# Kernel tuning notes

Hardware: AMD Instinct MI355X
Metric: run time of the kernel (lower is better)

Reference implementation:

```python
import jax, jax.numpy as jnp
import numpy as np
import math

N = 50000      # nodes (single node type 'mapping_var')
D = 128        # in_feats
R = 3          # relations
E = 800000     # edges per relation
OUT = 64
ALPHA = 0.5
BETA1 = math.log(2.0)    # log(lambda/layer + 1), layer=1, lambda=1
BETA2 = math.log(1.5)    # layer=2
SLOPE = 0.01             # leaky_relu default negative slope


def setup_inputs() -> dict:
    key = jax.random.key(0)
    ks = jax.random.split(key, 8)
    x = jax.random.normal(ks[0], (N, D), dtype=jnp.float32)
    src = jax.random.randint(ks[1], (R, E), 0, N, dtype=jnp.int32)
    dst = jax.random.randint(ks[2], (R, E), 0, N, dtype=jnp.int32)
    W1 = jax.random.normal(ks[3], (R, D, D), dtype=jnp.float32) * 0.05
    b1 = jnp.zeros((R, D), dtype=jnp.float32)
    W2 = jax.random.normal(ks[4], (R, D, D), dtype=jnp.float32) * 0.05
    b2 = jnp.zeros((R, D), dtype=jnp.float32)
    Wlin = jax.random.normal(ks[5], (D, OUT), dtype=jnp.float32) * 0.05
    blin = jnp.zeros((OUT,), dtype=jnp.float32)
    return {"x": x, "src": src, "dst": dst, "W1": W1, "b1": b1,
            "W2": W2, "b2": b2, "Wlin": Wlin, "blin": blin}


def _gcn2_rel(h, feat0, src, dst, W, b, beta, act):
    """One GCN2Conv on one relation. h,feat0: [N,D]; src,dst: [E]."""
    ones = jnp.ones(src.shape, h.dtype)
    deg_out = jnp.maximum(jax.ops.segment_sum(ones, src, num_segments=N), 1.0)
    deg_in = jnp.maximum(jax.ops.segment_sum(ones, dst, num_segments=N), 1.0)
    hs = h * (deg_out ** -0.5)[:, None]              # src-side normalize
    agg = jax.ops.segment_sum(hs[src], dst, num_segments=N)  # SpMM via gather+scatter
    feat = agg * (deg_in ** -0.5)[:, None]           # dst-side normalize
    rst = feat * (1.0 - ALPHA) + ALPHA * feat0       # initial-residual blend
    rst = (1.0 - beta) * rst + beta * (rst @ W) + b  # identity mapping (project_initial_features)
    if act:
        rst = jnp.where(rst >= 0, rst, SLOPE * rst)  # leaky_relu
    return rst


def reference(x, src, dst, W1, b1, W2, b2, Wlin, blin):
    # conv1: per-relation GCN2Conv(layer=1, leaky_relu), mean-aggregate over relations
    h1 = jax.vmap(lambda s, d, w, bb: _gcn2_rel(x, x, s, d, w, bb, BETA1, True))(
        src, dst, W1, b1).mean(axis=0)
    # dropout: eval-mode identity
    # conv2: per-relation GCN2Conv(layer=2, no activation), feat_0 = original inputs
    h2 = jax.vmap(lambda s, d, w, bb: _gcn2_rel(h1, x, s, d, w, bb, BETA2, False))(
        src, dst, W2, b2).mean(axis=0)
    return h2 @ Wlin + blin
```

## Files before the change

### kernel.cpp

```cpp
#include <hip/hip_runtime.h>

#define NN    50000
#define DD    128
#define RR    3
#define EE    800000
#define OUTD  64
#define BKT   128
#define NBK   391
#define CAP   2560
#define CAPB  2560
#define CHUNK 2048
#define NCH   391
#define NPB   3125
#define ALPHA_ 0.5f
#define SLOPE_ 0.01f
#define BETA1_ 0.6931471805599453f
#define BETA2_ 0.4054651081081644f

typedef __attribute__((ext_vector_type(8))) short short8;
typedef __attribute__((ext_vector_type(4))) float f32x4;

__device__ __forceinline__ unsigned short f2b(float f) {
    unsigned int u = __builtin_bit_cast(unsigned int, f);
    u += 0x7FFFu + ((u >> 16) & 1u);
    return (unsigned short)(u >> 16);
}
__device__ __forceinline__ unsigned int pack2(float lo, float hi) {
    return (unsigned int)f2b(lo) | ((unsigned int)f2b(hi) << 16);
}
__device__ __forceinline__ float blo(unsigned int w) { return __builtin_bit_cast(float, w << 16); }
__device__ __forceinline__ float bhi(unsigned int w) { return __builtin_bit_cast(float, w & 0xFFFF0000u); }

__global__ __launch_bounds__(256) void bin_kernel(
    const int* __restrict__ src, const int* __restrict__ dst,
    int* __restrict__ bcnt_d, int* __restrict__ bcnt_s,
    int* __restrict__ pairs_d, unsigned short* __restrict__ pairs_s)
{
    __shared__ int hist[NBK];
    __shared__ int lbase[NBK];
    __shared__ int gdelta[NBK];
    __shared__ int lcur[NBK];
    __shared__ unsigned int staging[CHUNK];
    unsigned short* staging16 = (unsigned short*)staging;
    const int tid = threadIdx.x;
    const int r = blockIdx.x / NCH;
    const int chunk = blockIdx.x % NCH;
    const int e0 = chunk * CHUNK;
    const int n = min(CHUNK, EE - e0);
    const int* sp = src + (size_t)r * EE + e0;
    const int* dp = dst + (size_t)r * EE + e0;

    for (int i = tid; i < NBK; i += 256) hist[i] = 0;
    __syncthreads();
    for (int i = tid; i < n; i += 256)
        atomicAdd(&hist[dp[i] >> 7], 1);
    __syncthreads();
    if (tid < 64) {
        int carry = 0;
        for (int c0 = 0; c0 < NBK; c0 += 64) {
            const int idx = c0 + tid;
            const int v = (idx < NBK) ? hist[idx] : 0;
            int incl = v;
            #pragma unroll
            for (int d = 1; d < 64; d <<= 1) {
                const int t = __shfl_up(incl, d, 64);
                if (tid >= d) incl += t;
            }
            if (idx < NBK) lbase[idx] = carry + incl - v;
            carry += __shfl(incl, 63, 64);
        }
    }
    __syncthreads();
    for (int b = tid; b < NBK; b += 256) {
        lcur[b] = lbase[b];
        const int h = hist[b];
        if (h > 0) {
            const int gstart = (r * NBK + b) * CAP + atomicAdd(&bcnt_d[r * NBK + b], h);
            gdelta[b] = gstart - lbase[b];
        }
    }
    __syncthreads();
    for (int i = tid; i < n; i += 256) {
        const int d = dp[i];
        const int b = d >> 7;
        const int pos = atomicAdd(&lcur[b], 1);
        staging[pos] = (unsigned int)sp[i] | ((unsigned int)(d & 127) << 16)
                     | ((unsigned int)b << 23);
    }
    __syncthreads();
    for (int j = tid; j < n; j += 256) {
        const unsigned int v = staging[j];
        const int b = v >> 23;
        const int gi = gdelta[b] + j;
        const int lo = gi - (r * NBK + b) * CAP;
        if (lo < CAP) pairs_d[gi] = (int)(v & 0x7FFFFF);
    }
    __syncthreads();

    for (int i = tid; i < NBK; i += 256) hist[i] = 0;
    __syncthreads();
    for (int i = tid; i < n; i += 256)
        atomicAdd(&hist[sp[i] >> 7], 1);
    __syncthreads();
    if (tid < 64) {
        int carry = 0;
        for (int c0 = 0; c0 < NBK; c0 += 64) {
            const int idx = c0 + tid;
            const int v = (idx < NBK) ? hist[idx] : 0;
            int incl = v;
            #pragma unroll
            for (int d = 1; d < 64; d <<= 1) {
                const int t = __shfl_up(incl, d, 64);
                if (tid >= d) incl += t;
            }
            if (idx < NBK) lbase[idx] = carry + incl - v;
            carry += __shfl(incl, 63, 64);
        }
    }
    __syncthreads();
    for (int b = tid; b < NBK; b += 256) {
        lcur[b] = lbase[b];
        const int h = hist[b];
        if (h > 0) {
            const int gstart = (r * NBK + b) * CAPB + atomicAdd(&bcnt_s[r * NBK + b], h);
            gdelta[b] = gstart - lbase[b];
        }
    }
    __syncthreads();
    for (int i = tid; i < n; i += 256) {
        const int s = sp[i];
        const int b = s >> 7;
        const int pos = atomicAdd(&lcur[b], 1);
        staging16[pos] = (unsigned short)((b << 7) | (s & 127));
    }
    __syncthreads();
    for (int j = tid; j < n; j += 256) {
        const unsigned short v = staging16[j];
        const int b = v >> 7;
        const int gi = gdelta[b] + j;
        const int lo = gi - (r * NBK + b) * CAPB;
        if (lo < CAPB) pairs_s[gi] = v;
    }
}

__global__ __launch_bounds__(256) void sort_count_kernel(
    int* __restrict__ pairs_d, const unsigned short* __restrict__ pairs_s,
    const int* __restrict__ bcnt_d, const int* __restrict__ bcnt_s,
    int* __restrict__ off_g, int* __restrict__ cnt_g,
    float* __restrict__ degi_r, float* __restrict__ dego_r)
{
    __shared__ int stage[CAP];
    __shared__ int cnt[BKT];
    __shared__ int base[BKT];
    __shared__ int pos[BKT];
    __shared__ int scnt[BKT];
    const int tid = threadIdx.x;
    const int bid = blockIdx.x;
    const int n = min(bcnt_d[bid], CAP);
    const int n2 = min(bcnt_s[bid], CAPB);
    int* pp = pairs_d + (size_t)bid * CAP;
    const unsigned short* ps = pairs_s + (size_t)bid * CAPB;
    if (tid < BKT) { cnt[tid] = 0; scnt[tid] = 0; }
    __syncthreads();
    for (int i = tid; i < n; i += 256) {
        const int p = pp[i];
        stage[i] = p;
        atomicAdd(&cnt[p >> 16], 1);
    }
    for (int i = tid; i < n2; i += 256)
        atomicAdd(&scnt[ps[i] & 127], 1);
    __syncthreads();
    if (tid < 64) {
        int carry = 0;
        for (int c0 = 0; c0 < BKT; c0 += 64) {
            const int v = cnt[c0 + tid];
            int incl = v;
            #pragma unroll
            for (int d = 1; d < 64; d <<= 1) {
                const int t = __shfl_up(incl, d, 64);
                if (tid >= d) incl += t;
            }
            base[c0 + tid] = carry + incl - v;
            carry += __shfl(incl, 63, 64);
        }
    }
    __syncthreads();
    if (tid < BKT) {
        pos[tid] = base[tid];
        const int r = bid / NBK;
        const int g = (bid % NBK) * BKT + tid;
        if (g < NN) {
            off_g[r * NN + g] = bid * CAP + base[tid];
            cnt_g[r * NN + g] = cnt[tid];
            degi_r[r * NN + g] = rsqrtf((float)max(cnt[tid], 1));
            dego_r[r * NN + g] = rsqrtf((float)max(scnt[tid], 1));
        }
    }
    __syncthreads();
    for (int i = tid; i < n; i += 256) {
        const int p = stage[i];
        const int q = atomicAdd(&pos[p >> 16], 1);
        pp[q] = p & 0xFFFF;
    }
}

__global__ __launch_bounds__(256) void setup_kernel(
    const float* __restrict__ x, unsigned short* __restrict__ xb,
    const float* __restrict__ W1, const float* __restrict__ W2,
    const float* __restrict__ Wlin, unsigned short* __restrict__ Wt1,
    unsigned short* __restrict__ Wt2, unsigned short* __restrict__ WlT)
{
    const int i = blockIdx.x * 256 + threadIdx.x;
    {
        const float4 v = ((const float4*)x)[i];
        ushort4 o;
        o.x = f2b(v.x); o.y = f2b(v.y); o.z = f2b(v.z); o.w = f2b(v.w);
        ((ushort4*)xb)[i] = o;
    }
    if (i < RR * DD * DD) {
        const int r = i >> 14, rem = i & 16383, nn = rem >> 7, k = rem & 127;
        const float diag = (k == nn) ? 1.0f : 0.0f;
        const float w1 = W1[r * DD * DD + k * DD + nn];
        Wt1[i] = f2b(BETA1_ * w1 + diag * (1.0f - BETA1_));
        const float w2 = W2[r * DD * DD + k * DD + nn];
        Wt2[i] = f2b((BETA2_ * w2 + diag * (1.0f - BETA2_)) * (1.0f / 3.0f));
    } else if (i < RR * DD * DD + OUTD * DD) {
        const int j = i - RR * DD * DD;
        const int nn = j >> 7, k = j & 127;
        WlT[j] = f2b(Wlin[k * OUTD + nn]);
    }
}

__global__ __launch_bounds__(256) void pull_all_kernel(
    const unsigned short* __restrict__ hb,
    const unsigned short* __restrict__ xb,
    const int* __restrict__ pairs, const int* __restrict__ off_g,
    const int* __restrict__ cnt_g, const float* __restrict__ dego_r,
    const float* __restrict__ degi_r, unsigned short* __restrict__ aggb)
{
    const int blk = blockIdx.x;
    const int r = blk / NPB;
    const int node = (blk % NPB) * 16 + (threadIdx.x >> 4);
    const int lane = threadIdx.x & 15;
    const int gi = r * NN + node;
    const int j0 = off_g[gi];
    const int j1 = j0 + cnt_g[gi];
    const float* dego = dego_r + (size_t)r * NN;
    const uint4* hb4 = (const uint4*)hb;
    float a0 = 0.f, a1 = 0.f, a2 = 0.f, a3 = 0.f, a4 = 0.f, a5 = 0.f, a6 = 0.f, a7 = 0.f;
    int j = j0;
    for (; j + 4 <= j1; j += 4) {
        const int s0 = pairs[j], s1 = pairs[j + 1], s2 = pairs[j + 2], s3 = pairs[j + 3];
        const float n0 = dego[s0], n1 = dego[s1], n2 = dego[s2], n3 = dego[s3];
        const uint4 q0 = hb4[(size_t)s0 * 16 + lane];
        const uint4 q1 = hb4[(size_t)s1 * 16 + lane];
        const uint4 q2 = hb4[(size_t)s2 * 16 + lane];
        const uint4 q3 = hb4[(size_t)s3 * 16 + lane];
        a0 += blo(q0.x) * n0 + blo(q1.x) * n1 + blo(q2.x) * n2 + blo(q3.x) * n3;
        a1 += bhi(q0.x) * n0 + bhi(q1.x) * n1 + bhi(q2.x) * n2 + bhi(q3.x) * n3;
        a2 += blo(q0.y) * n0 + blo(q1.y) * n1 + blo(q2.y) * n2 + blo(q3.y) * n3;
        a3 += bhi(q0.y) * n0 + bhi(q1.y) * n1 + bhi(q2.y) * n2 + bhi(q3.y) * n3;
        a4 += blo(q0.z) * n0 + blo(q1.z) * n1 + blo(q2.z) * n2 + blo(q3.z) * n3;
        a5 += bhi(q0.z) * n0 + bhi(q1.z) * n1 + bhi(q2.z) * n2 + bhi(q3.z) * n3;
        a6 += blo(q0.w) * n0 + blo(q1.w) * n1 + blo(q2.w) * n2 + blo(q3.w) * n3;
        a7 += bhi(q0.w) * n0 + bhi(q1.w) * n1 + bhi(q2.w) * n2 + bhi(q3.w) * n3;
    }
    for (; j < j1; ++j) {
        const int s0 = pairs[j];
        const float n0 = dego[s0];
        const uint4 q0 = hb4[(size_t)s0 * 16 + lane];
        a0 += blo(q0.x) * n0; a1 += bhi(q0.x) * n0;
        a2 += blo(q0.y) * n0; a3 += bhi(q0.y) * n0;
        a4 += blo(q0.z) * n0; a5 += bhi(q0.z) * n0;
        a6 += blo(q0.w) * n0; a7 += bhi(q0.w) * n0;
    }
    const float nd = degi_r[gi] * (1.0f - ALPHA_);
    const uint4 xq = ((const uint4*)xb)[(size_t)node * 16 + lane];
    uint4 o;
    o.x = pack2(a0 * nd + ALPHA_ * blo(xq.x), a1 * nd + ALPHA_ * bhi(xq.x));
    o.y = pack2(a2 * nd + ALPHA_ * blo(xq.y), a3 * nd + ALPHA_ * bhi(xq.y));
    o.z = pack2(a4 * nd + ALPHA_ * blo(xq.z), a5 * nd + ALPHA_ * bhi(xq.z));
    o.w = pack2(a6 * nd + ALPHA_ * blo(xq.w), a7 * nd + ALPHA_ * bhi(xq.w));
    ((uint4*)aggb)[(size_t)gi * 16 + lane] = o;
}

template<int LIN>
__global__ __launch_bounds__(256) void conv_mfma_kernel(
    const unsigned short* __restrict__ aggb,
    const unsigned short* __restrict__ WtG,
    const float* __restrict__ bias,
    const unsigned short* __restrict__ WlT,
    const float* __restrict__ blin,
    unsigned short* __restrict__ houtb,
    float* __restrict__ outf)
{
    __shared__ unsigned short WtL[DD * 136];
    uint4* WtL4 = (uint4*)WtL;
    const int tid  = threadIdx.x;
    const int wave = tid >> 6;
    const int lane = tid & 63;
    const int l15  = lane & 15;
    const int q    = lane >> 4;
    const int blockRow = blockIdx.x * 64;
    const int row0 = blockRow + wave * 16;
    const int arow = min(row0 + l15, NN - 1);

    f32x4 o[8];
    if (LIN) {
        #pragma unroll
        for (int ct = 0; ct < 8; ++ct) {
            const int col = ct * 16 + l15;
            const float bv = (bias[col] + bias[DD + col] + bias[2 * DD + col]) * (1.0f / 3.0f);
            o[ct] = (f32x4){bv, bv, bv, bv};
        }
    } else {
        #pragma unroll
        for (int ct = 0; ct < 8; ++ct) o[ct] = (f32x4){0.f, 0.f, 0.f, 0.f};
    }

    for (int r = 0; r < RR; ++r) {
        __syncthreads();
        const uint4* wg = (const uint4*)(WtG + (size_t)r * DD * DD);
        for (int i = tid; i < DD * 16; i += 256)
            WtL4[(i >> 4) * 17 + (i & 15)] = wg[i];
        __syncthreads();

        short8 a[4];
        const uint4* ap = (const uint4*)aggb + ((size_t)r * NN + arow) * 16 + q;
        #pragma unroll
        for (int ks = 0; ks < 4; ++ks)
            a[ks] = __builtin_bit_cast(short8, ap[ks * 4]);

        #pragma unroll
        for (int ct = 0; ct < 8; ++ct) {
            f32x4 acc;
            if (LIN) {
                acc = o[ct];
            } else {
                const float bv = bias[r * DD + ct * 16 + l15];
                acc = (f32x4){bv, bv, bv, bv};
            }
            const int nrow = ct * 16 + l15;
            #pragma unroll
            for (int ks = 0; ks < 4; ++ks) {
                const short8 b = __builtin_bit_cast(short8, WtL4[nrow * 17 + ks * 4 + q]);
                acc = __builtin_amdgcn_mfma_f32_16x16x32_bf16(a[ks], b, acc, 0, 0, 0);
            }
            if (LIN) {
                o[ct] = acc;
            } else {
                #pragma unroll
                for (int e = 0; e < 4; ++e) {
                    float v = acc[e];
                    v = v >= 0.f ? v : SLOPE_ * v;
                    o[ct][e] += v * (1.0f / 3.0f);
                }
            }
        }
    }

    __syncthreads();
    unsigned short* tile = WtL;
    #pragma unroll
    for (int ct = 0; ct < 8; ++ct) {
        const int col = ct * 16 + l15;
        #pragma unroll
        for (int e = 0; e < 4; ++e) {
            const int lrow = wave * 16 + q * 4 + e;
            tile[lrow * 136 + col] = f2b(o[ct][e]);
        }
    }
    if (LIN) {
        uint4* wl4 = WtL4 + 64 * 17;
        const uint4* wg = (const uint4*)WlT;
        for (int i = tid; i < OUTD * 16; i += 256)
            wl4[(i >> 4) * 17 + (i & 15)] = wg[i];
    }
    __syncthreads();

    if (!LIN) {
        for (int i = tid; i < 64 * 16; i += 256) {
            const int lrow = i >> 4, c = i & 15;
            const int grow = blockRow + lrow;
            if (grow < NN)
                ((uint4*)houtb)[(size_t)grow * 16 + c] = WtL4[lrow * 17 + c];
        }
    } else {
        short8 a2[4];
        const int lrow = wave * 16 + l15;
        #pragma unroll
        for (int ks = 0; ks < 4; ++ks)
            a2[ks] = __builtin_bit_cast(short8, WtL4[lrow * 17 + ks * 4 + q]);
        #pragma unroll
        for (int ct = 0; ct < 4; ++ct) {
            const int col = ct * 16 + l15;
            const float bv = blin[col];
            f32x4 acc = (f32x4){bv, bv, bv, bv};
            #pragma unroll
            for (int ks = 0; ks < 4; ++ks) {
                const short8 b = __builtin_bit_cast(short8, WtL4[(64 + col) * 17 + ks * 4 + q]);
                acc = __builtin_amdgcn_mfma_f32_16x16x32_bf16(a2[ks], b, acc, 0, 0, 0);
            }
            #pragma unroll
            for (int e = 0; e < 4; ++e) {
                const int grow = row0 + q * 4 + e;
                if (grow < NN) outf[(size_t)grow * OUTD + col] = acc[e];
            }
        }
    }
}

extern "C" void kernel_launch(void* const* d_in, const int* in_sizes, int n_in,
                              void* d_out, int out_size, void* d_ws, size_t ws_size,
                              hipStream_t stream)
{
    const float* x    = (const float*)d_in[0];
    const int*   src  = (const int*)  d_in[1];
    const int*   dst  = (const int*)  d_in[2];
    const float* W1   = (const float*)d_in[3];
    const float* b1   = (const float*)d_in[4];
    const float* W2   = (const float*)d_in[5];
    const float* b2   = (const float*)d_in[6];
    const float* Wlin = (const float*)d_in[7];
    const float* blin = (const float*)d_in[8];
    float* out = (float*)d_out;

    int*   bcnt_d  = (int*)d_ws;
    int*   bcnt_s  = bcnt_d + RR * NBK;
    float* dego_r  = (float*)(bcnt_s + RR * NBK);
    float* degi_r  = dego_r + RR * NN;
    int*   off_g   = (int*)(degi_r + RR * NN);
    int*   cnt_g   = off_g + RR * NN;
    int*   pairs_d = cnt_g + RR * NN;
    unsigned short* pairs_s = (unsigned short*)(pairs_d + (size_t)RR * NBK * CAP);
    unsigned short* xb   = pairs_s + (size_t)RR * NBK * CAPB;
    unsigned short* h1b  = xb + (size_t)NN * DD;
    unsigned short* aggb = h1b + (size_t)NN * DD;
    unsigned short* Wt1  = aggb + (size_t)RR * NN * DD;
    unsigned short* Wt2  = Wt1 + RR * DD * DD;
    unsigned short* WlT  = Wt2 + RR * DD * DD;

    hipMemsetAsync(bcnt_d, 0, (size_t)2 * RR * NBK * sizeof(int), stream);

    const int gemm_blocks = (NN + 63) / 64;

    bin_kernel<<<RR * NCH, 256, 0, stream>>>(src, dst, bcnt_d, bcnt_s, pairs_d, pairs_s);
    setup_kernel<<<NN * DD / 4 / 256, 256, 0, stream>>>(
        x, xb, W1, W2, Wlin, Wt1, Wt2, WlT);
    sort_count_kernel<<<RR * NBK, 256, 0, stream>>>(
        pairs_d, pairs_s, bcnt_d, bcnt_s, off_g, cnt_g, degi_r, dego_r);

    pull_all_kernel<<<RR * NPB, 256, 0, stream>>>(
        xb, xb, pairs_d, off_g, cnt_g, dego_r, degi_r, aggb);
    conv_mfma_kernel<0><<<gemm_blocks, 256, 0, stream>>>(
        aggb, Wt1, b1, nullptr, nullptr, h1b, nullptr);

    pull_all_kernel<<<RR * NPB, 256, 0, stream>>>(
        h1b, xb, pairs_d, off_g, cnt_g, dego_r, degi_r, aggb);
    conv_mfma_kernel<1><<<gemm_blocks, 256, 0, stream>>>(
        aggb, Wt2, b2, WlT, blin, nullptr, out);
}
```

Baseline: 416.2 us.

## Split node features into column chunks for cache-resident SpMM gathers

Stores x and h1 as four column-chunked bf16 tables (32 features per node per chunk), so each pull block gathers from a 3.2 MB table that fits in cache better than the full 12.8 MB one. Each block now handles one chunk for 64 nodes and walks all three relations, with 4 lanes per node instead of 16. A 48 KB dynamic LDS pad is added to cap occupancy and reduce cache thrashing. The trade-off is that every edge list and degree value is re-read once per chunk, and each gather request is narrower.

```diff
diff --git a/kernel.cpp b/kernel.cpp
--- a/kernel.cpp
+++ b/kernel.cpp
@@ -11,7 +11,8 @@
 #define CAPB  2560
 #define CHUNK 2048
 #define NCH   391
-#define NPB   3125
+#define NCK   4
+#define NNB   782
 #define ALPHA_ 0.5f
 #define SLOPE_ 0.01f
 #define BETA1_ 0.6931471805599453f
@@ -205,17 +206,19 @@
 }
 
 __global__ __launch_bounds__(256) void setup_kernel(
-    const float* __restrict__ x, unsigned short* __restrict__ xb,
+    const float* __restrict__ x, unsigned short* __restrict__ xbc,
     const float* __restrict__ W1, const float* __restrict__ W2,
     const float* __restrict__ Wlin, unsigned short* __restrict__ Wt1,
     unsigned short* __restrict__ Wt2, unsigned short* __restrict__ WlT)
 {
     const int i = blockIdx.x * 256 + threadIdx.x;
     {
+        const int node = i >> 5, j = i & 31;
+        const int c = j >> 3, jj = j & 7;
         const float4 v = ((const float4*)x)[i];
         ushort4 o;
         o.x = f2b(v.x); o.y = f2b(v.y); o.z = f2b(v.z); o.w = f2b(v.w);
-        ((ushort4*)xb)[i] = o;
+        ((ushort4*)xbc)[((size_t)c * NN + node) * 8 + jj] = o;
     }
     if (i < RR * DD * DD) {
         const int r = i >> 14, rem = i & 16383, nn = rem >> 7, k = rem & 127;
@@ -231,57 +234,64 @@
     }
 }
 
-__global__ __launch_bounds__(256) void pull_all_kernel(
-    const unsigned short* __restrict__ hb,
-    const unsigned short* __restrict__ xb,
+__global__ __launch_bounds__(256) void pull_chunk_kernel(
+    const uint4* __restrict__ hbc,
+    const uint4* __restrict__ xbc,
     const int* __restrict__ pairs, const int* __restrict__ off_g,
     const int* __restrict__ cnt_g, const float* __restrict__ dego_r,
-    const float* __restrict__ degi_r, unsigned short* __restrict__ aggb)
-{
+    const float* __restrict__ degi_r, uint4* __restrict__ aggb4)
+{
+    extern __shared__ char occ_pad[];
     const int blk = blockIdx.x;
-    const int r = blk / NPB;
-    const int node = (blk % NPB) * 16 + (threadIdx.x >> 4);
-    const int lane = threadIdx.x & 15;
-    const int gi = r * NN + node;
-    const int j0 = off_g[gi];
-    const int j1 = j0 + cnt_g[gi];
-    const float* dego = dego_r + (size_t)r * NN;
-    const uint4* hb4 = (const uint4*)hb;
-    float a0 = 0.f, a1 = 0.f, a2 = 0.f, a3 = 0.f, a4 = 0.f, a5 = 0.f, a6 = 0.f, a7 = 0.f;
-    int j = j0;
-    for (; j + 4 <= j1; j += 4) {
-        const int s0 = pairs[j], s1 = pairs[j + 1], s2 = pairs[j + 2], s3 = pairs[j + 3];
-        const float n0 = dego[s0], n1 = dego[s1], n2 = dego[s2], n3 = dego[s3];
-        const uint4 q0 = hb4[(size_t)s0 * 16 + lane];
-        const uint4 q1 = hb4[(size_t)s1 * 16 + lane];
-        const uint4 q2 = hb4[(size_t)s2 * 16 + lane];
-        const uint4 q3 = hb4[(size_t)s3 * 16 + lane];
-        a0 += blo(q0.x) * n0 + blo(q1.x) * n1 + blo(q2.x) * n2 + blo(q3.x) * n3;
-        a1 += bhi(q0.x) * n0 + bhi(q1.x) * n1 + bhi(q2.x) * n2 + bhi(q3.x) * n3;
-        a2 += blo(q0.y) * n0 + blo(q1.y) * n1 + blo(q2.y) * n2 + blo(q3.y) * n3;
-        a3 += bhi(q0.y) * n0 + bhi(q1.y) * n1 + bhi(q2.y) * n2 + bhi(q3.y) * n3;
-        a4 += blo(q0.z) * n0 + blo(q1.z) * n1 + blo(q2.z) * n2 + blo(q3.z) * n3;
-        a5 += bhi(q0.z) * n0 + bhi(q1.z) * n1 + bhi(q2.z) * n2 + bhi(q3.z) * n3;
-        a6 += blo(q0.w) * n0 + blo(q1.w) * n1 + blo(q2.w) * n2 + blo(q3.w) * n3;
-        a7 += bhi(q0.w) * n0 + bhi(q1.w) * n1 + bhi(q2.w) * n2 + bhi(q3.w) * n3;
-    }
-    for (; j < j1; ++j) {
-        const int s0 = pairs[j];
-        const float n0 = dego[s0];
-        const uint4 q0 = hb4[(size_t)s0 * 16 + lane];
-        a0 += blo(q0.x) * n0; a1 += bhi(q0.x) * n0;
-        a2 += blo(q0.y) * n0; a3 += bhi(q0.y) * n0;
-        a4 += blo(q0.z) * n0; a5 += bhi(q0.z) * n0;
-        a6 += blo(q0.w) * n0; a7 += bhi(q0.w) * n0;
-    }
-    const float nd = degi_r[gi] * (1.0f - ALPHA_);
-    const uint4 xq = ((const uint4*)xb)[(size_t)node * 16 + lane];
-    uint4 o;
-    o.x = pack2(a0 * nd + ALPHA_ * blo(xq.x), a1 * nd + ALPHA_ * bhi(xq.x));
-    o.y = pack2(a2 * nd + ALPHA_ * blo(xq.y), a3 * nd + ALPHA_ * bhi(xq.y));
-    o.z = pack2(a4 * nd + ALPHA_ * blo(xq.z), a5 * nd + ALPHA_ * bhi(xq.z));
-    o.w = pack2(a6 * nd + ALPHA_ * blo(xq.w), a7 * nd + ALPHA_ * bhi(xq.w));
-    ((uint4*)aggb)[(size_t)gi * 16 + lane] = o;
+    const int c = blk / NNB;
+    const int nb = blk % NNB;
+    const int group = threadIdx.x >> 2;
+    const int lane = threadIdx.x & 3;
+    const int node = nb * 64 + group;
+    if (node >= NN) return;
+    const uint4* table = hbc + (size_t)c * NN * 4 + lane;
+    const uint4 xq = xbc[((size_t)c * NN + node) * 4 + lane];
+
+    for (int r = 0; r < RR; ++r) {
+        const int gi = r * NN + node;
+        const int n = cnt_g[gi];
+        const int* pp = pairs + off_g[gi];
+        const float* dego = dego_r + (size_t)r * NN;
+        float a0 = 0.f, a1 = 0.f, a2 = 0.f, a3 = 0.f, a4 = 0.f, a5 = 0.f, a6 = 0.f, a7 = 0.f;
+        int e = 0;
+        for (; e + 4 <= n; e += 4) {
+            const int s0 = pp[e], s1 = pp[e + 1], s2 = pp[e + 2], s3 = pp[e + 3];
+            const float n0 = dego[s0], n1 = dego[s1], n2 = dego[s2], n3 = dego[s3];
+            const uint4 q0 = table[(size_t)s0 * 4];
+            const uint4 q1 = table[(size_t)s1 * 4];
+            const uint4 q2 = table[(size_t)s2 * 4];
+            const uint4 q3 = table[(size_t)s3 * 4];
+            a0 += blo(q0.x) * n0 + blo(q1.x) * n1 + blo(q2.x) * n2 + blo(q3.x) * n3;
+            a1 += bhi(q0.x) * n0 + bhi(q1.x) * n1 + bhi(q2.x) * n2 + bhi(q3.x) * n3;
+            a2 += blo(q0.y) * n0 + blo(q1.y) * n1 + blo(q2.y) * n2 + blo(q3.y) * n3;
+            a3 += bhi(q0.y) * n0 + bhi(q1.y) * n1 + bhi(q2.y) * n2 + bhi(q3.y) * n3;
+            a4 += blo(q0.z) * n0 + blo(q1.z) * n1 + blo(q2.z) * n2 + blo(q3.z) * n3;
+            a5 += bhi(q0.z) * n0 + bhi(q1.z) * n1 + bhi(q2.z) * n2 + bhi(q3.z) * n3;
+            a6 += blo(q0.w) * n0 + blo(q1.w) * n1 + blo(q2.w) * n2 + blo(q3.w) * n3;
+            a7 += bhi(q0.w) * n0 + bhi(q1.w) * n1 + bhi(q2.w) * n2 + bhi(q3.w) * n3;
+        }
+        for (; e < n; ++e) {
+            const int s0 = pp[e];
+            const float n0 = dego[s0];
+            const uint4 q0 = table[(size_t)s0 * 4];
+            a0 += blo(q0.x) * n0; a1 += bhi(q0.x) * n0;
+            a2 += blo(q0.y) * n0; a3 += bhi(q0.y) * n0;
+            a4 += blo(q0.z) * n0; a5 += bhi(q0.z) * n0;
+            a6 += blo(q0.w) * n0; a7 += bhi(q0.w) * n0;
+        }
+        const float nd = degi_r[gi] * (1.0f - ALPHA_);
+        uint4 o;
+        o.x = pack2(a0 * nd + ALPHA_ * blo(xq.x), a1 * nd + ALPHA_ * bhi(xq.x));
+        o.y = pack2(a2 * nd + ALPHA_ * blo(xq.y), a3 * nd + ALPHA_ * bhi(xq.y));
+        o.z = pack2(a4 * nd + ALPHA_ * blo(xq.z), a5 * nd + ALPHA_ * bhi(xq.z));
+        o.w = pack2(a6 * nd + ALPHA_ * blo(xq.w), a7 * nd + ALPHA_ * bhi(xq.w));
+        aggb4[(size_t)gi * 16 + c * 4 + lane] = o;
+    }
 }
 
 template<int LIN>
@@ -291,7 +301,7 @@
     const float* __restrict__ bias,
     const unsigned short* __restrict__ WlT,
     const float* __restrict__ blin,
-    unsigned short* __restrict__ houtb,
+    uint4* __restrict__ h1bc4,
     float* __restrict__ outf)
 {
     __shared__ unsigned short WtL[DD * 136];
@@ -380,10 +390,10 @@
 
     if (!LIN) {
         for (int i = tid; i < 64 * 16; i += 256) {
-            const int lrow = i >> 4, c = i & 15;
+            const int lrow = i >> 4, cc = i & 15;
             const int grow = blockRow + lrow;
             if (grow < NN)
-                ((uint4*)houtb)[(size_t)grow * 16 + c] = WtL4[lrow * 17 + c];
+                h1bc4[((size_t)(cc >> 2) * NN + grow) * 4 + (cc & 3)] = WtL4[lrow * 17 + cc];
         }
     } else {
         short8 a2[4];
@@ -431,11 +441,11 @@
     float* degi_r  = dego_r + RR * NN;
     int*   off_g   = (int*)(degi_r + RR * NN);
     int*   cnt_g   = off_g + RR * NN;
-    int*   pairs_d = cnt_g + RR * NN;
+    int*   pairs_d = cnt_g + RR * NN + 2;
     unsigned short* pairs_s = (unsigned short*)(pairs_d + (size_t)RR * NBK * CAP);
-    unsigned short* xb   = pairs_s + (size_t)RR * NBK * CAPB;
-    unsigned short* h1b  = xb + (size_t)NN * DD;
-    unsigned short* aggb = h1b + (size_t)NN * DD;
+    unsigned short* xbc  = pairs_s + (size_t)RR * NBK * CAPB;
+    unsigned short* h1bc = xbc + (size_t)NN * DD;
+    unsigned short* aggb = h1bc + (size_t)NN * DD;
     unsigned short* Wt1  = aggb + (size_t)RR * NN * DD;
     unsigned short* Wt2  = Wt1 + RR * DD * DD;
     unsigned short* WlT  = Wt2 + RR * DD * DD;
@@ -443,20 +453,23 @@
     hipMemsetAsync(bcnt_d, 0, (size_t)2 * RR * NBK * sizeof(int), stream);
 
     const int gemm_blocks = (NN + 63) / 64;
+    const int PAD_LDS = 49152;
 
     bin_kernel<<<RR * NCH, 256, 0, stream>>>(src, dst, bcnt_d, bcnt_s, pairs_d, pairs_s);
     setup_kernel<<<NN * DD / 4 / 256, 256, 0, stream>>>(
-        x, xb, W1, W2, Wlin, Wt1, Wt2, WlT);
+        x, xbc, W1, W2, Wlin, Wt1, Wt2, WlT);
     sort_count_kernel<<<RR * NBK, 256, 0, stream>>>(
         pairs_d, pairs_s, bcnt_d, bcnt_s, off_g, cnt_g, degi_r, dego_r);
 
-    pull_all_kernel<<<RR * NPB, 256, 0, stream>>>(
-        xb, xb, pairs_d, off_g, cnt_g, dego_r, degi_r, aggb);
+    pull_chunk_kernel<<<NCK * NNB, 256, PAD_LDS, stream>>>(
+        (const uint4*)xbc, (const uint4*)xbc, pairs_d, off_g, cnt_g,
+        dego_r, degi_r, (uint4*)aggb);
     conv_mfma_kernel<0><<<gemm_blocks, 256, 0, stream>>>(
-        aggb, Wt1, b1, nullptr, nullptr, h1b, nullptr);
-
-    pull_all_kernel<<<RR * NPB, 256, 0, stream>>>(
-        h1b, xb, pairs_d, off_g, cnt_g, dego_r, degi_r, aggb);
+        aggb, Wt1, b1, nullptr, nullptr, (uint4*)h1bc, nullptr);
+
+    pull_chunk_kernel<<<NCK * NNB, 256, PAD_LDS, stream>>>(
+        (const uint4*)h1bc, (const uint4*)xbc, pairs_d, off_g, cnt_g,
+        dego_r, degi_r, (uint4*)aggb);
     conv_mfma_kernel<1><<<gemm_blocks, 256, 0, stream>>>(
         aggb, Wt2, b2, WlT, blin, nullptr, out);
 }
```

After: 526.3 us. +26.5%, slower.
